# Optimization experiments

Measured on AMD Instinct MI355X. Metric: run time of the kernel, lower is better.

The kernel has to match this reference:

```python
import jax, jax.numpy as jnp
import numpy as np

N, F, E = 100000, 128, 1600000


def setup_inputs() -> dict:
    key = jax.random.key(0)
    ks = jax.random.split(key, 10)
    s = 1.0 / np.sqrt(F)
    return {
        "x": jax.random.normal(ks[0], (N, F), jnp.float32),
        "edge_index": jax.random.randint(ks[1], (2, E), 0, N),
        "edge_weight": jax.random.uniform(ks[2], (E,), jnp.float32),
        # EvolveGCNO initial weight (1, F, F) -> squeezed to (F, F)
        "initial_weight": jax.random.normal(ks[3], (F, F), jnp.float32) * s,
        # torch.nn.GRU(F, F) params, gate order (r, z, n)
        "gru_w_ih": jax.random.uniform(ks[4], (3 * F, F), jnp.float32, -s, s),
        "gru_w_hh": jax.random.uniform(ks[5], (3 * F, F), jnp.float32, -s, s),
        "gru_b_ih": jax.random.uniform(ks[6], (3 * F,), jnp.float32, -s, s),
        "gru_b_hh": jax.random.uniform(ks[7], (3 * F,), jnp.float32, -s, s),
        # Linear(F, 1)
        "lin_w": jax.random.uniform(ks[8], (1, F), jnp.float32, -s, s),
        "lin_b": jax.random.uniform(ks[9], (1,), jnp.float32, -s, s),
    }


def _evolve_weight(W0, w_ih, w_hh, b_ih, b_hh):
    # One GRU step: input = W0 rows (batch=F), hidden = W0 rows (first call of EvolveGCNO)
    gi = W0 @ w_ih.T + b_ih  # (F, 3F)
    gh = W0 @ w_hh.T + b_hh
    i_r, i_z, i_n = jnp.split(gi, 3, axis=-1)
    h_r, h_z, h_n = jnp.split(gh, 3, axis=-1)
    r = jax.nn.sigmoid(i_r + h_r)
    z = jax.nn.sigmoid(i_z + h_z)
    n = jnp.tanh(i_n + r * h_n)
    return (1.0 - z) * n + z * W0  # (F, F)


def reference(x, edge_index, edge_weight, initial_weight, gru_w_ih, gru_w_hh,
              gru_b_ih, gru_b_hh, lin_w, lin_b):
    W = _evolve_weight(initial_weight, gru_w_ih, gru_w_hh, gru_b_ih, gru_b_hh)
    n_nodes = x.shape[0]
    row, col = edge_index[0], edge_index[1]  # source, target
    # gcn_norm: add self loops (weight 1), sym-normalize D^-1/2 (A+I) D^-1/2
    loop = jnp.arange(n_nodes)
    row = jnp.concatenate([row, loop])
    col = jnp.concatenate([col, loop])
    w = jnp.concatenate([edge_weight, jnp.ones((n_nodes,), x.dtype)])
    deg = jax.ops.segment_sum(w, col, num_segments=n_nodes)
    dinv = jnp.where(deg > 0, jax.lax.rsqrt(deg), 0.0)
    norm = dinv[row] * w * dinv[col]  # (E+N,)
    xw = x @ W  # (N, F)
    # gather at sources, weighted scatter-add at targets
    h = jax.ops.segment_sum(norm[:, None] * xw[row], col, num_segments=n_nodes)
    h = jax.nn.relu(h)
    return (h @ lin_w.T + lin_b)[:, 0]  # (N,)
```

## Files before the change

kernel.cpp:

```cpp
#include <hip/hip_runtime.h>

#define F 128
#define DEG_SCALE 16777216.0f
#define DEG_INV   (1.0f / 16777216.0f)
#define BUCK_BITS 7
#define BUCK_COLS 128
#define CAP 2304
#define EPT 8
#define WB_STRIDE 136

typedef _Float16 half8 __attribute__((ext_vector_type(8)));
typedef float f32x4 __attribute__((ext_vector_type(4)));

__global__ __launch_bounds__(256) void init_kernel(
    int* __restrict__ cursor, int NZ, int NBUK,
    const float* __restrict__ W0, const float* __restrict__ wih,
    const float* __restrict__ whh, const float* __restrict__ bih,
    const float* __restrict__ bhh, _Float16* __restrict__ WTh,
    int* __restrict__ offs, uint2* __restrict__ pairs, int N, int total) {
  __shared__ float wrow[6 * F];
  int b = blockIdx.x;
  int tid = threadIdx.x;
  if (b < NZ) {
    int i = b * 256 + tid;
    if (i < NBUK) cursor[i] = 0;
    if (b == 0) {
      if (tid < 16) pairs[total + tid] = make_uint2(0u, 0u);
      if (tid == 0) offs[N] = total;
    }
    return;
  }
  int j = b - NZ;
  for (int idx = tid; idx < 6 * F; idx += 256) {
    int g = idx >> 7, k = idx & 127;
    const float* src = (g < 3) ? (wih + (size_t)(g * F + j) * F)
                               : (whh + (size_t)((g - 3) * F + j) * F);
    wrow[idx] = src[k];
  }
  __syncthreads();
  int i = tid >> 1;
  int kh = tid & 1;
  const float* w0p = W0 + (size_t)i * F + kh * 64;
  const float* wr = wrow + kh * 64;
  float ar = 0, az = 0, an = 0, br = 0, bz = 0, bn = 0;
#pragma unroll 4
  for (int k = 0; k < 64; ++k) {
    float a = w0p[k];
    ar = fmaf(a, wr[k], ar);
    az = fmaf(a, wr[F + k], az);
    an = fmaf(a, wr[2 * F + k], an);
    br = fmaf(a, wr[3 * F + k], br);
    bz = fmaf(a, wr[4 * F + k], bz);
    bn = fmaf(a, wr[5 * F + k], bn);
  }
  ar += __shfl_xor(ar, 1); az += __shfl_xor(az, 1); an += __shfl_xor(an, 1);
  br += __shfl_xor(br, 1); bz += __shfl_xor(bz, 1); bn += __shfl_xor(bn, 1);
  if (kh == 0) {
    float gr = ar + bih[j] + br + bhh[j];
    float gz = az + bih[j + F] + bz + bhh[j + F];
    float r = 1.f / (1.f + expf(-gr));
    float z = 1.f / (1.f + expf(-gz));
    float n = tanhf(an + bih[j + 2 * F] + r * (bn + bhh[j + 2 * F]));
    float v = (1.f - z) * n + z * W0[(size_t)i * F + j];
    WTh[(size_t)j * F + i] = (_Float16)v;
  }
}

__global__ __launch_bounds__(1024) void bin_kernel(
    const int* __restrict__ row, const int* __restrict__ col,
    const float* __restrict__ ew, int* __restrict__ cursor,
    uint2* __restrict__ binned, int E, int NBUK) {
  __shared__ int cnt[1024];
  __shared__ int base[1024];
  int tid = threadIdx.x;
  cnt[tid] = 0;
  __syncthreads();
  int e0 = blockIdx.x * (1024 * EPT) + tid;
  int cc[EPT];
  int lrank[EPT];
#pragma unroll
  for (int k = 0; k < EPT; ++k) {
    int e = e0 + k * 1024;
    if (e < E) {
      cc[k] = col[e];
      lrank[k] = atomicAdd(&cnt[cc[k] >> BUCK_BITS], 1);
    } else cc[k] = -1;
  }
  __syncthreads();
  if (tid < NBUK) {
    int c = cnt[tid];
    base[tid] = c ? atomicAdd(&cursor[tid], c) : 0;
  }
  __syncthreads();
#pragma unroll
  for (int k = 0; k < EPT; ++k) {
    if (cc[k] >= 0) {
      int e = e0 + k * 1024;
      int b = cc[k] >> BUCK_BITS;
      int pos = base[b] + lrank[k];
      if (pos < CAP) {
        unsigned cl = (unsigned)(cc[k] & (BUCK_COLS - 1));
        binned[(size_t)b * CAP + pos] =
            make_uint2((unsigned)row[e] | (cl << 17), __float_as_uint(ew[e]));
      }
    }
  }
}

__global__ __launch_bounds__(256) void csr_deg(
    const uint2* __restrict__ binned, const int* __restrict__ cursor,
    int* __restrict__ offs, float* __restrict__ dinv, int N, int NBUK) {
  __shared__ unsigned long long acc[BUCK_COLS];
  __shared__ int sc[BUCK_COLS];
  __shared__ int wsum[4];
  int b = blockIdx.x;
  int tid = threadIdx.x;
  if (tid < BUCK_COLS) acc[tid] = 0ull;
  int partial = 0;
  for (int i = tid; i < b; i += 256) partial += cursor[i];
#pragma unroll
  for (int m = 32; m; m >>= 1) partial += __shfl_xor(partial, m);
  if ((tid & 63) == 0) wsum[tid >> 6] = partial;
  __syncthreads();
  int bstart = b * BUCK_COLS + wsum[0] + wsum[1] + wsum[2] + wsum[3];

  int cnt = cursor[b];
  if (cnt > CAP) cnt = CAP;
  const uint2* src = binned + (size_t)b * CAP;
  for (int i = tid; i < cnt; i += 256) {
    uint2 rec = src[i];
    int cl = rec.x >> 17;
    unsigned fx = (unsigned)(__uint_as_float(rec.y) * DEG_SCALE);
    atomicAdd(&acc[cl], ((unsigned long long)1 << 32) | (unsigned long long)fx);
  }
  __syncthreads();
  int node0 = b * BUCK_COLS;
  int cvt1 = 0;
  if (tid < BUCK_COLS) {
    unsigned long long pk = acc[tid];
    int node = node0 + tid;
    if (node < N) {
      cvt1 = (int)(pk >> 32) + 1;
      float deg = (float)(unsigned)(pk & 0xffffffffull) * DEG_INV;
      float dv = rsqrtf(deg + 1.0f);
      dinv[node] = dv;
    }
    sc[tid] = cvt1;
  }
  __syncthreads();
  for (int off = 1; off < BUCK_COLS; off <<= 1) {
    int xv = 0;
    if (tid < BUCK_COLS && tid >= off) xv = sc[tid - off];
    __syncthreads();
    if (tid < BUCK_COLS) sc[tid] += xv;
    __syncthreads();
  }
  if (tid < BUCK_COLS) {
    int node = node0 + tid;
    if (node < N) offs[node] = bstart + sc[tid] - cvt1;
  }
}

__global__ __launch_bounds__(256) void csr_pairs(
    const uint2* __restrict__ binned, const int* __restrict__ cursor,
    const int* __restrict__ offs, const float* __restrict__ dinv,
    uint2* __restrict__ pairs, int N, int NBUK) {
  __shared__ float dinvL[BUCK_COLS];
  __shared__ int wbase[BUCK_COLS];
  int b = blockIdx.x;
  int tid = threadIdx.x;
  int node0 = b * BUCK_COLS;
  if (tid < BUCK_COLS) {
    int node = node0 + tid;
    if (node < N) {
      int o = offs[node];
      float dv = dinv[node];
      dinvL[tid] = dv;
      wbase[tid] = o + 1;
      pairs[o] = make_uint2((unsigned)node << 8, __float_as_uint(dv * dv));
    }
  }
  __syncthreads();
  int cnt = cursor[b];
  if (cnt > CAP) cnt = CAP;
  const uint2* src = binned + (size_t)b * CAP;
  for (int i = tid; i < cnt; i += 256) {
    uint2 rec = src[i];
    int cl = rec.x >> 17;
    unsigned r = rec.x & 0x1ffffu;
    float wp = (__uint_as_float(rec.y) * dinvL[cl]) * dinv[r];
    int pos = atomicAdd(&wbase[cl], 1);
    pairs[pos] = make_uint2(r << 8, __float_as_uint(wp));
  }
}

__global__ __launch_bounds__(256) void gemm_xw(
    const float* __restrict__ x, const _Float16* __restrict__ WT,
    _Float16* __restrict__ xwh, int N) {
  __shared__ _Float16 Wb[F * WB_STRIDE];
  int t = threadIdx.x;
  for (int idx = t; idx < F * F; idx += 256) {
    int n = idx >> 7, k = idx & 127;
    Wb[n * WB_STRIDE + k] = WT[idx];
  }
  __syncthreads();

  int lane = t & 63, wave = t >> 6;
  int ln = lane & 15, q = lane >> 4;
  int rowb = blockIdx.x * 64 + wave * 16;
  int i = rowb + ln;
  int iclamp = (i < N) ? i : N - 1;
  const float* xp = x + (size_t)iclamp * F + q * 8;

  half8 a[4];
#pragma unroll
  for (int tt = 0; tt < 4; ++tt) {
    float4 v0 = *(const float4*)(xp + 32 * tt);
    float4 v1 = *(const float4*)(xp + 32 * tt + 4);
    half8 av;
    av[0] = (_Float16)v0.x; av[1] = (_Float16)v0.y;
    av[2] = (_Float16)v0.z; av[3] = (_Float16)v0.w;
    av[4] = (_Float16)v1.x; av[5] = (_Float16)v1.y;
    av[6] = (_Float16)v1.z; av[7] = (_Float16)v1.w;
    a[tt] = av;
  }

  f32x4 acc[8];
#pragma unroll
  for (int nt = 0; nt < 8; ++nt) acc[nt] = (f32x4){0.f, 0.f, 0.f, 0.f};

#pragma unroll
  for (int nt = 0; nt < 8; ++nt) {
#pragma unroll
    for (int tt = 0; tt < 4; ++tt) {
      half8 bfrag = *(const half8*)&Wb[(nt * 16 + ln) * WB_STRIDE + tt * 32 + q * 8];
      acc[nt] = __builtin_amdgcn_mfma_f32_16x16x32_f16(a[tt], bfrag, acc[nt], 0, 0, 0);
    }
  }

#pragma unroll
  for (int nt = 0; nt < 8; ++nt) {
#pragma unroll
    for (int r = 0; r < 4; ++r) {
      int rowi = rowb + q * 4 + r;
      if (rowi < N) xwh[(size_t)rowi * F + nt * 16 + ln] = (_Float16)acc[nt][r];
    }
  }
}

__global__ __launch_bounds__(256) void gather_out(
    const uint2* __restrict__ pairs, const int* __restrict__ offs,
    const char* __restrict__ xwb, const float* __restrict__ linw,
    const float* __restrict__ linb, float* __restrict__ out, int N) {
  int wave = threadIdx.x >> 6;
  int lane = threadIdx.x & 63;
  int node = blockIdx.x * 4 + wave;
  if (node >= N) return;
  int c = lane & 15;
  int q = lane >> 4;

  const char* xb = xwb + (c << 4);
  float acc[8];
#pragma unroll
  for (int j = 0; j < 8; ++j) acc[j] = 0.f;

  int start = offs[node], end = offs[node + 1];
  for (int it = start + q; it < end; it += 16) {
    uint2 p0 = pairs[it];
    uint2 p1 = pairs[it + 4];
    uint2 p2 = pairs[it + 8];
    uint2 p3 = pairs[it + 12];
    float n0 = __uint_as_float(p0.y);
    float n1 = (it + 4 < end) ? __uint_as_float(p1.y) : 0.f;
    float n2 = (it + 8 < end) ? __uint_as_float(p2.y) : 0.f;
    float n3 = (it + 12 < end) ? __uint_as_float(p3.y) : 0.f;
    half8 x0 = *(const half8*)(xb + p0.x);
    half8 x1 = *(const half8*)(xb + p1.x);
    half8 x2 = *(const half8*)(xb + p2.x);
    half8 x3 = *(const half8*)(xb + p3.x);
#pragma unroll
    for (int j = 0; j < 8; ++j) acc[j] = fmaf(n0, (float)x0[j], acc[j]);
#pragma unroll
    for (int j = 0; j < 8; ++j) acc[j] = fmaf(n1, (float)x1[j], acc[j]);
#pragma unroll
    for (int j = 0; j < 8; ++j) acc[j] = fmaf(n2, (float)x2[j], acc[j]);
#pragma unroll
    for (int j = 0; j < 8; ++j) acc[j] = fmaf(n3, (float)x3[j], acc[j]);
  }

#pragma unroll
  for (int j = 0; j < 8; ++j) {
    acc[j] += __shfl_xor(acc[j], 16);
    acc[j] += __shfl_xor(acc[j], 32);
  }

  const float4* lw4 = (const float4*)linw;
  float4 la = lw4[c * 2];
  float4 lb = lw4[c * 2 + 1];
  float p = fmaxf(acc[0], 0.f) * la.x + fmaxf(acc[1], 0.f) * la.y +
            fmaxf(acc[2], 0.f) * la.z + fmaxf(acc[3], 0.f) * la.w +
            fmaxf(acc[4], 0.f) * lb.x + fmaxf(acc[5], 0.f) * lb.y +
            fmaxf(acc[6], 0.f) * lb.z + fmaxf(acc[7], 0.f) * lb.w;
#pragma unroll
  for (int m = 8; m; m >>= 1) p += __shfl_xor(p, m);

  if (lane == 0) out[node] = p + linb[0];
}

extern "C" void kernel_launch(void* const* d_in, const int* in_sizes, int n_in,
                              void* d_out, int out_size, void* d_ws, size_t ws_size,
                              hipStream_t stream) {
  const float* x    = (const float*)d_in[0];
  const int*   ei   = (const int*)d_in[1];
  const float* ew   = (const float*)d_in[2];
  const float* W0   = (const float*)d_in[3];
  const float* wih  = (const float*)d_in[4];
  const float* whh  = (const float*)d_in[5];
  const float* bih  = (const float*)d_in[6];
  const float* bhh  = (const float*)d_in[7];
  const float* linw = (const float*)d_in[8];
  const float* linb = (const float*)d_in[9];

  int N = in_sizes[0] / F;
  int E = in_sizes[2];
  const int* row = ei;
  const int* col = ei + E;
  int NBUK = (N + BUCK_COLS - 1) / BUCK_COLS;
  int total = E + N;

  char* p = (char*)d_ws;
  auto alloc = [&](size_t bytes) {
    char* q = p;
    p += (bytes + 255) & ~(size_t)255;
    return q;
  };
  _Float16* WTh    = (_Float16*)alloc((size_t)F * F * 2);
  int*      cursor = (int*)alloc((size_t)NBUK * 4);
  float*    dinv   = (float*)alloc((size_t)N * 4);
  int*      offs   = (int*)alloc(((size_t)N + 1) * 4);
  uint2*    binned = (uint2*)alloc((size_t)NBUK * CAP * 8);
  uint2*    pairs  = (uint2*)alloc(((size_t)total + 16) * 8);
  _Float16* xwh    = (_Float16*)alloc((size_t)N * F * 2);

  int NZ = (NBUK + 255) / 256;
  init_kernel<<<NZ + 128, 256, 0, stream>>>(cursor, NZ, NBUK, W0, wih, whh, bih,
                                            bhh, WTh, offs, pairs, N, total);

  int EPB = 1024 * EPT;
  bin_kernel<<<(E + EPB - 1) / EPB, 1024, 0, stream>>>(row, col, ew, cursor, binned,
                                                       E, NBUK);
  csr_deg<<<NBUK, 256, 0, stream>>>(binned, cursor, offs, dinv, N, NBUK);
  csr_pairs<<<NBUK, 256, 0, stream>>>(binned, cursor, offs, dinv, pairs, N, NBUK);

  gemm_xw<<<(N + 63) / 64, 256, 0, stream>>>(x, WTh, xwh, N);
  gather_out<<<(N + 3) / 4, 256, 0, stream>>>(pairs, offs, (const char*)xwh,
                                              linw, linb, (float*)d_out, N);
}
```

Measured before the change: 228.7 us.

## Merge edge binning and XW GEMM into one interleaved launch

Replaces the separate bin_kernel and gemm_xw launches with a single kernel whose blocks are interleaved: every third block bins edges into column buckets and the other two compute a 64-row tile of x@W with MFMA. The aim is to overlap the atomic-heavy, memory-bound binning with the GEMM and to drop one launch, letting the GEMM finish before the CSR passes. Binning blocks now use 256 threads handling 2048 edges each instead of 1024 threads handling 8192, which means more blocks and more global cursor atomics. Shared memory is sized for the GEMM's W tile, so binning blocks carry the same LDS footprint.

```diff
diff --git a/kernel.cpp b/kernel.cpp
--- a/kernel.cpp
+++ b/kernel.cpp
@@ -66,43 +66,103 @@
   }
 }
 
-__global__ __launch_bounds__(1024) void bin_kernel(
-    const int* __restrict__ row, const int* __restrict__ col,
+__global__ __launch_bounds__(256) void gemm_bin(
+    const float* __restrict__ x, const _Float16* __restrict__ WT,
+    _Float16* __restrict__ xwh, int N, int NG,
+    const int* __restrict__ erow, const int* __restrict__ ecol,
     const float* __restrict__ ew, int* __restrict__ cursor,
-    uint2* __restrict__ binned, int E, int NBUK) {
-  __shared__ int cnt[1024];
-  __shared__ int base[1024];
-  int tid = threadIdx.x;
-  cnt[tid] = 0;
-  __syncthreads();
-  int e0 = blockIdx.x * (1024 * EPT) + tid;
-  int cc[EPT];
-  int lrank[EPT];
-#pragma unroll
-  for (int k = 0; k < EPT; ++k) {
-    int e = e0 + k * 1024;
-    if (e < E) {
-      cc[k] = col[e];
-      lrank[k] = atomicAdd(&cnt[cc[k] >> BUCK_BITS], 1);
-    } else cc[k] = -1;
-  }
-  __syncthreads();
-  if (tid < NBUK) {
-    int c = cnt[tid];
-    base[tid] = c ? atomicAdd(&cursor[tid], c) : 0;
-  }
-  __syncthreads();
-#pragma unroll
-  for (int k = 0; k < EPT; ++k) {
-    if (cc[k] >= 0) {
-      int e = e0 + k * 1024;
-      int b = cc[k] >> BUCK_BITS;
-      int pos = base[b] + lrank[k];
-      if (pos < CAP) {
-        unsigned cl = (unsigned)(cc[k] & (BUCK_COLS - 1));
-        binned[(size_t)b * CAP + pos] =
-            make_uint2((unsigned)row[e] | (cl << 17), __float_as_uint(ew[e]));
+    uint2* __restrict__ binned, int E, int NBUK, int NBIN) {
+  __shared__ __align__(16) char smem[F * WB_STRIDE * 2];
+  int bi = blockIdx.x;
+  if (bi % 3 == 2) {
+    int bb = bi / 3;
+    if (bb >= NBIN) return;
+    int* cnt = (int*)smem;
+    int* base = cnt + 1024;
+    int tid = threadIdx.x;
+    for (int u = tid; u < 1024; u += 256) cnt[u] = 0;
+    __syncthreads();
+    int e0 = bb * (256 * EPT) + tid;
+    int cc[EPT];
+    int lrank[EPT];
+#pragma unroll
+    for (int k = 0; k < EPT; ++k) {
+      int e = e0 + k * 256;
+      if (e < E) {
+        cc[k] = ecol[e];
+        lrank[k] = atomicAdd(&cnt[cc[k] >> BUCK_BITS], 1);
+      } else cc[k] = -1;
+    }
+    __syncthreads();
+    for (int u = tid; u < NBUK; u += 256) {
+      int cu = cnt[u];
+      base[u] = cu ? atomicAdd(&cursor[u], cu) : 0;
+    }
+    __syncthreads();
+#pragma unroll
+    for (int k = 0; k < EPT; ++k) {
+      if (cc[k] >= 0) {
+        int e = e0 + k * 256;
+        int bk = cc[k] >> BUCK_BITS;
+        int pos = base[bk] + lrank[k];
+        if (pos < CAP) {
+          unsigned cl = (unsigned)(cc[k] & (BUCK_COLS - 1));
+          binned[(size_t)bk * CAP + pos] =
+              make_uint2((unsigned)erow[e] | (cl << 17), __float_as_uint(ew[e]));
+        }
       }
+    }
+    return;
+  }
+  int g = (bi / 3) * 2 + (bi % 3);
+  if (g >= NG) return;
+  _Float16* Wb = (_Float16*)smem;
+  int t = threadIdx.x;
+  for (int idx = t; idx < F * F; idx += 256) {
+    int n = idx >> 7, k = idx & 127;
+    Wb[n * WB_STRIDE + k] = WT[idx];
+  }
+  __syncthreads();
+
+  int lane = t & 63, wave = t >> 6;
+  int ln = lane & 15, q = lane >> 4;
+  int rowb = g * 64 + wave * 16;
+  int i = rowb + ln;
+  int iclamp = (i < N) ? i : N - 1;
+  const float* xp = x + (size_t)iclamp * F + q * 8;
+
+  half8 a[4];
+#pragma unroll
+  for (int tt = 0; tt < 4; ++tt) {
+    float4 v0 = *(const float4*)(xp + 32 * tt);
+    float4 v1 = *(const float4*)(xp + 32 * tt + 4);
+    half8 av;
+    av[0] = (_Float16)v0.x; av[1] = (_Float16)v0.y;
+    av[2] = (_Float16)v0.z; av[3] = (_Float16)v0.w;
+    av[4] = (_Float16)v1.x; av[5] = (_Float16)v1.y;
+    av[6] = (_Float16)v1.z; av[7] = (_Float16)v1.w;
+    a[tt] = av;
+  }
+
+  f32x4 acc[8];
+#pragma unroll
+  for (int nt = 0; nt < 8; ++nt) acc[nt] = (f32x4){0.f, 0.f, 0.f, 0.f};
+
+#pragma unroll
+  for (int nt = 0; nt < 8; ++nt) {
+#pragma unroll
+    for (int tt = 0; tt < 4; ++tt) {
+      half8 bfrag = *(const half8*)&Wb[(nt * 16 + ln) * WB_STRIDE + tt * 32 + q * 8];
+      acc[nt] = __builtin_amdgcn_mfma_f32_16x16x32_f16(a[tt], bfrag, acc[nt], 0, 0, 0);
+    }
+  }
+
+#pragma unroll
+  for (int nt = 0; nt < 8; ++nt) {
+#pragma unroll
+    for (int r = 0; r < 4; ++r) {
+      int rowi = rowb + q * 4 + r;
+      if (rowi < N) xwh[(size_t)rowi * F + nt * 16 + ln] = (_Float16)acc[nt][r];
     }
   }
 }
@@ -194,60 +254,6 @@
   }
 }
 
-__global__ __launch_bounds__(256) void gemm_xw(
-    const float* __restrict__ x, const _Float16* __restrict__ WT,
-    _Float16* __restrict__ xwh, int N) {
-  __shared__ _Float16 Wb[F * WB_STRIDE];
-  int t = threadIdx.x;
-  for (int idx = t; idx < F * F; idx += 256) {
-    int n = idx >> 7, k = idx & 127;
-    Wb[n * WB_STRIDE + k] = WT[idx];
-  }
-  __syncthreads();
-
-  int lane = t & 63, wave = t >> 6;
-  int ln = lane & 15, q = lane >> 4;
-  int rowb = blockIdx.x * 64 + wave * 16;
-  int i = rowb + ln;
-  int iclamp = (i < N) ? i : N - 1;
-  const float* xp = x + (size_t)iclamp * F + q * 8;
-
-  half8 a[4];
-#pragma unroll
-  for (int tt = 0; tt < 4; ++tt) {
-    float4 v0 = *(const float4*)(xp + 32 * tt);
-    float4 v1 = *(const float4*)(xp + 32 * tt + 4);
-    half8 av;
-    av[0] = (_Float16)v0.x; av[1] = (_Float16)v0.y;
-    av[2] = (_Float16)v0.z; av[3] = (_Float16)v0.w;
-    av[4] = (_Float16)v1.x; av[5] = (_Float16)v1.y;
-    av[6] = (_Float16)v1.z; av[7] = (_Float16)v1.w;
-    a[tt] = av;
-  }
-
-  f32x4 acc[8];
-#pragma unroll
-  for (int nt = 0; nt < 8; ++nt) acc[nt] = (f32x4){0.f, 0.f, 0.f, 0.f};
-
-#pragma unroll
-  for (int nt = 0; nt < 8; ++nt) {
-#pragma unroll
-    for (int tt = 0; tt < 4; ++tt) {
-      half8 bfrag = *(const half8*)&Wb[(nt * 16 + ln) * WB_STRIDE + tt * 32 + q * 8];
-      acc[nt] = __builtin_amdgcn_mfma_f32_16x16x32_f16(a[tt], bfrag, acc[nt], 0, 0, 0);
-    }
-  }
-
-#pragma unroll
-  for (int nt = 0; nt < 8; ++nt) {
-#pragma unroll
-    for (int r = 0; r < 4; ++r) {
-      int rowi = rowb + q * 4 + r;
-      if (rowi < N) xwh[(size_t)rowi * F + nt * 16 + ln] = (_Float16)acc[nt][r];
-    }
-  }
-}
-
 __global__ __launch_bounds__(256) void gather_out(
     const uint2* __restrict__ pairs, const int* __restrict__ offs,
     const char* __restrict__ xwb, const float* __restrict__ linw,
@@ -346,13 +352,16 @@
   init_kernel<<<NZ + 128, 256, 0, stream>>>(cursor, NZ, NBUK, W0, wih, whh, bih,
                                             bhh, WTh, offs, pairs, N, total);
 
-  int EPB = 1024 * EPT;
-  bin_kernel<<<(E + EPB - 1) / EPB, 1024, 0, stream>>>(row, col, ew, cursor, binned,
-                                                       E, NBUK);
+  int NG = (N + 63) / 64;
+  int NBIN = (E + 256 * EPT - 1) / (256 * EPT);
+  int half_g = (NG + 1) / 2;
+  int G3 = NBIN > half_g ? NBIN : half_g;
+  gemm_bin<<<3 * G3, 256, 0, stream>>>(x, WTh, xwh, N, NG, row, col, ew, cursor,
+                                       binned, E, NBUK, NBIN);
+
   csr_deg<<<NBUK, 256, 0, stream>>>(binned, cursor, offs, dinv, N, NBUK);
   csr_pairs<<<NBUK, 256, 0, stream>>>(binned, cursor, offs, dinv, pairs, N, NBUK);
 
-  gemm_xw<<<(N + 63) / 64, 256, 0, stream>>>(x, WTh, xwh, N);
   gather_out<<<(N + 3) / 4, 256, 0, stream>>>(pairs, offs, (const char*)xwh,
                                               linw, linb, (float*)d_out, N);
 }
```

After: 239.9 us. +4.9%, slower.

## Fold degree normalization into GEMM and gather, fuse CSR degree and pair kernels

Applied to the files above, without the earlier changes.

Factors the symmetric normalization so source-side dinv scales rows of xW in the GEMM epilogue and target-side dinv scales the aggregated sum in gather_out. Pairs then store the raw edge weight, which lets the degree and pair-building kernels merge into one. Each thread keeps its binned records in registers (up to 9) between the two phases. This removes one launch, a second read of the binned array, and the random dinv[r] gathers. In exchange the fp16 xw values are now prescaled by dinv, which shifts rounding slightly, and the register array adds pressure.

```diff
diff --git a/kernel.cpp b/kernel.cpp
--- a/kernel.cpp
+++ b/kernel.cpp
@@ -107,11 +107,13 @@
   }
 }
 
-__global__ __launch_bounds__(256) void csr_deg(
+__global__ __launch_bounds__(256) void csr_fused(
     const uint2* __restrict__ binned, const int* __restrict__ cursor,
-    int* __restrict__ offs, float* __restrict__ dinv, int N, int NBUK) {
+    int* __restrict__ offs, float* __restrict__ dinv,
+    uint2* __restrict__ pairs, int N, int NBUK) {
   __shared__ unsigned long long acc[BUCK_COLS];
   __shared__ int sc[BUCK_COLS];
+  __shared__ int wbase[BUCK_COLS];
   __shared__ int wsum[4];
   int b = blockIdx.x;
   int tid = threadIdx.x;
@@ -127,11 +129,14 @@
   int cnt = cursor[b];
   if (cnt > CAP) cnt = CAP;
   const uint2* src = binned + (size_t)b * CAP;
+  uint2 rec[9];
+  int nr = 0;
   for (int i = tid; i < cnt; i += 256) {
-    uint2 rec = src[i];
-    int cl = rec.x >> 17;
-    unsigned fx = (unsigned)(__uint_as_float(rec.y) * DEG_SCALE);
-    atomicAdd(&acc[cl], ((unsigned long long)1 << 32) | (unsigned long long)fx);
+    rec[nr] = src[i];
+    unsigned fx = (unsigned)(__uint_as_float(rec[nr].y) * DEG_SCALE);
+    atomicAdd(&acc[rec[nr].x >> 17],
+              ((unsigned long long)1 << 32) | (unsigned long long)fx);
+    ++nr;
   }
   __syncthreads();
   int node0 = b * BUCK_COLS;
@@ -142,8 +147,7 @@
     if (node < N) {
       cvt1 = (int)(pk >> 32) + 1;
       float deg = (float)(unsigned)(pk & 0xffffffffull) * DEG_INV;
-      float dv = rsqrtf(deg + 1.0f);
-      dinv[node] = dv;
+      dinv[node] = rsqrtf(deg + 1.0f);
     }
     sc[tid] = cvt1;
   }
@@ -157,46 +161,25 @@
   }
   if (tid < BUCK_COLS) {
     int node = node0 + tid;
-    if (node < N) offs[node] = bstart + sc[tid] - cvt1;
-  }
-}
-
-__global__ __launch_bounds__(256) void csr_pairs(
-    const uint2* __restrict__ binned, const int* __restrict__ cursor,
-    const int* __restrict__ offs, const float* __restrict__ dinv,
-    uint2* __restrict__ pairs, int N, int NBUK) {
-  __shared__ float dinvL[BUCK_COLS];
-  __shared__ int wbase[BUCK_COLS];
-  int b = blockIdx.x;
-  int tid = threadIdx.x;
-  int node0 = b * BUCK_COLS;
-  if (tid < BUCK_COLS) {
-    int node = node0 + tid;
     if (node < N) {
-      int o = offs[node];
-      float dv = dinv[node];
-      dinvL[tid] = dv;
-      wbase[tid] = o + 1;
-      pairs[o] = make_uint2((unsigned)node << 8, __float_as_uint(dv * dv));
-    }
-  }
-  __syncthreads();
-  int cnt = cursor[b];
-  if (cnt > CAP) cnt = CAP;
-  const uint2* src = binned + (size_t)b * CAP;
-  for (int i = tid; i < cnt; i += 256) {
-    uint2 rec = src[i];
-    int cl = rec.x >> 17;
-    unsigned r = rec.x & 0x1ffffu;
-    float wp = (__uint_as_float(rec.y) * dinvL[cl]) * dinv[r];
+      int abs0 = bstart + sc[tid] - cvt1;
+      offs[node] = abs0;
+      pairs[abs0] = make_uint2((unsigned)node << 8, __float_as_uint(1.0f));
+      wbase[tid] = abs0 + 1;
+    }
+  }
+  __syncthreads();
+  for (int k = 0; k < nr; ++k) {
+    int cl = rec[k].x >> 17;
+    unsigned r = rec[k].x & 0x1ffffu;
     int pos = atomicAdd(&wbase[cl], 1);
-    pairs[pos] = make_uint2(r << 8, __float_as_uint(wp));
+    pairs[pos] = make_uint2(r << 8, rec[k].y);
   }
 }
 
 __global__ __launch_bounds__(256) void gemm_xw(
     const float* __restrict__ x, const _Float16* __restrict__ WT,
-    _Float16* __restrict__ xwh, int N) {
+    const float* __restrict__ dinv, _Float16* __restrict__ xwh, int N) {
   __shared__ _Float16 Wb[F * WB_STRIDE];
   int t = threadIdx.x;
   for (int idx = t; idx < F * F; idx += 256) {
@@ -238,20 +221,28 @@
     }
   }
 
+  float dv[4];
+#pragma unroll
+  for (int r = 0; r < 4; ++r) {
+    int rowi = rowb + q * 4 + r;
+    dv[r] = (rowi < N) ? dinv[rowi] : 0.f;
+  }
 #pragma unroll
   for (int nt = 0; nt < 8; ++nt) {
 #pragma unroll
     for (int r = 0; r < 4; ++r) {
       int rowi = rowb + q * 4 + r;
-      if (rowi < N) xwh[(size_t)rowi * F + nt * 16 + ln] = (_Float16)acc[nt][r];
+      if (rowi < N)
+        xwh[(size_t)rowi * F + nt * 16 + ln] = (_Float16)(acc[nt][r] * dv[r]);
     }
   }
 }
 
 __global__ __launch_bounds__(256) void gather_out(
     const uint2* __restrict__ pairs, const int* __restrict__ offs,
-    const char* __restrict__ xwb, const float* __restrict__ linw,
-    const float* __restrict__ linb, float* __restrict__ out, int N) {
+    const float* __restrict__ dinv, const char* __restrict__ xwb,
+    const float* __restrict__ linw, const float* __restrict__ linb,
+    float* __restrict__ out, int N) {
   int wave = threadIdx.x >> 6;
   int lane = threadIdx.x & 63;
   int node = blockIdx.x * 4 + wave;
@@ -259,6 +250,7 @@
   int c = lane & 15;
   int q = lane >> 4;
 
+  float dvn = dinv[node];
   const char* xb = xwb + (c << 4);
   float acc[8];
 #pragma unroll
@@ -297,10 +289,10 @@
   const float4* lw4 = (const float4*)linw;
   float4 la = lw4[c * 2];
   float4 lb = lw4[c * 2 + 1];
-  float p = fmaxf(acc[0], 0.f) * la.x + fmaxf(acc[1], 0.f) * la.y +
-            fmaxf(acc[2], 0.f) * la.z + fmaxf(acc[3], 0.f) * la.w +
-            fmaxf(acc[4], 0.f) * lb.x + fmaxf(acc[5], 0.f) * lb.y +
-            fmaxf(acc[6], 0.f) * lb.z + fmaxf(acc[7], 0.f) * lb.w;
+  float p = fmaxf(dvn * acc[0], 0.f) * la.x + fmaxf(dvn * acc[1], 0.f) * la.y +
+            fmaxf(dvn * acc[2], 0.f) * la.z + fmaxf(dvn * acc[3], 0.f) * la.w +
+            fmaxf(dvn * acc[4], 0.f) * lb.x + fmaxf(dvn * acc[5], 0.f) * lb.y +
+            fmaxf(dvn * acc[6], 0.f) * lb.z + fmaxf(dvn * acc[7], 0.f) * lb.w;
 #pragma unroll
   for (int m = 8; m; m >>= 1) p += __shfl_xor(p, m);
 
@@ -349,10 +341,9 @@
   int EPB = 1024 * EPT;
   bin_kernel<<<(E + EPB - 1) / EPB, 1024, 0, stream>>>(row, col, ew, cursor, binned,
                                                        E, NBUK);
-  csr_deg<<<NBUK, 256, 0, stream>>>(binned, cursor, offs, dinv, N, NBUK);
-  csr_pairs<<<NBUK, 256, 0, stream>>>(binned, cursor, offs, dinv, pairs, N, NBUK);
-
-  gemm_xw<<<(N + 63) / 64, 256, 0, stream>>>(x, WTh, xwh, N);
-  gather_out<<<(N + 3) / 4, 256, 0, stream>>>(pairs, offs, (const char*)xwh,
+  csr_fused<<<NBUK, 256, 0, stream>>>(binned, cursor, offs, dinv, pairs, N, NBUK);
+
+  gemm_xw<<<(N + 63) / 64, 256, 0, stream>>>(x, WTh, dinv, xwh, N);
+  gather_out<<<(N + 3) / 4, 256, 0, stream>>>(pairs, offs, dinv, (const char*)xwh,
                                               linw, linb, (float*)d_out, N);
 }
```

Measured after the change: 229.3 us. About the same (+0.3%).
